# Kernel optimization log

Hardware: AMD Instinct MI355X
Metric: run time of the kernel (lower is better)

Reference implementation:

```python
import jax, jax.numpy as jnp
import numpy as np

DIM = 768
N_HEADS = 12
HEAD_DIM = DIM // N_HEADS  # 64
SEQ = 4096
ROPE_THETA = 10000.0  # local layer (layer_id=1)
WINDOW = 128          # local_attention; mask is distance <= WINDOW // 2


def setup_inputs() -> dict:
    key = jax.random.key(0)
    k1, k2, k3 = jax.random.split(key, 3)
    x = jax.random.normal(k1, (1, SEQ, DIM), dtype=jnp.float32)
    position_ids = jnp.arange(SEQ, dtype=jnp.int64 if jax.config.jax_enable_x64 else jnp.int32).reshape(1, SEQ)
    wqkv = jax.random.normal(k2, (3 * DIM, DIM), dtype=jnp.float32) * 0.02
    wo = jax.random.normal(k3, (DIM, DIM), dtype=jnp.float32) * 0.02
    return {"x": x, "position_ids": position_ids, "wqkv": wqkv, "wo": wo}


def _rope_cos_sin(position_ids):
    # inv_freq over even dims, freqs duplicated to full head_dim
    inv_freq = 1.0 / (ROPE_THETA ** (jnp.arange(0, HEAD_DIM, 2, dtype=jnp.float32) / HEAD_DIM))
    pos = position_ids.reshape(-1).astype(jnp.float32)           # [S]
    freqs = pos[:, None] * inv_freq[None, :]                      # [S, hd/2]
    freqs = jnp.concatenate([freqs, freqs], axis=-1)              # [S, hd]
    return jnp.cos(freqs)[None, None], jnp.sin(freqs)[None, None]  # [1,1,S,hd]


def _rotate_half(t):
    h = t.shape[-1] // 2
    return jnp.concatenate([-t[..., h:], t[..., :h]], axis=-1)


def reference(x, position_ids, wqkv, wo):
    bsz, seq_len, _ = x.shape
    qkv = jnp.einsum("bsd,ed->bse", x, wqkv)                      # [B,S,3*dim]
    qkv = qkv.reshape(bsz, seq_len, 3, N_HEADS, HEAD_DIM)
    qkv = jnp.transpose(qkv, (0, 3, 2, 1, 4))                      # [B,H,3,S,hd]
    q, k, v = qkv[:, :, 0], qkv[:, :, 1], qkv[:, :, 2]             # [B,H,S,hd]

    cos, sin = _rope_cos_sin(position_ids)
    q = q * cos + _rotate_half(q) * sin
    k = k * cos + _rotate_half(k) * sin

    scale = HEAD_DIM ** -0.5
    scores = jnp.einsum("bhqd,bhkd->bhqk", q, k) * scale           # [B,H,S,S]

    # sliding-window mask: |i - j| <= WINDOW // 2
    idx = jnp.arange(seq_len)
    dist = jnp.abs(idx[None, :] - idx[:, None])                    # [S,S]
    window_mask = dist <= (WINDOW // 2)
    scores = jnp.where(window_mask[None, None], scores, -jnp.inf)

    attn = jax.nn.softmax(scores, axis=-1)
    out = jnp.einsum("bhqk,bhkd->bhqd", attn, v)                   # [B,H,S,hd]
    out = jnp.transpose(out, (0, 2, 1, 3)).reshape(bsz, seq_len, DIM)
    out = jnp.einsum("bsd,ed->bse", out, wo)
    return out
```

## Files before the change

### kernel.cpp

```cpp
#include <hip/hip_runtime.h>
#include <math.h>

#define SEQ 4096
#define DIM 768
#define NH 12
#define HD 64
#define QKV_N 2304
#define HALF_WIN 64

typedef __attribute__((ext_vector_type(8))) short bf16x8;
typedef __attribute__((ext_vector_type(4))) float floatx4;

__device__ __forceinline__ unsigned short f2bf(float f) {
    unsigned u = __float_as_uint(f);
    unsigned r = (u + 0x7fffu + ((u >> 16) & 1u)) >> 16;
    return (unsigned short)r;
}

__device__ __forceinline__ void gld16(const void* g, void* l) {
    __builtin_amdgcn_global_load_lds(
        (const __attribute__((address_space(1))) unsigned*)g,
        (__attribute__((address_space(3))) unsigned*)l, 16, 0, 0);
}

__device__ __forceinline__ void fast_sc(float x, float* s, float* c) {
    float r = x * 0.15915494309189535f;
    r = r - floorf(r);
    *s = __builtin_amdgcn_sinf(r);
    *c = __builtin_amdgcn_cosf(r);
}

__global__ __launch_bounds__(256) void cast3_bf16(const float* __restrict__ x,
                                                  const float* __restrict__ wqkv,
                                                  const float* __restrict__ wo,
                                                  unsigned short* __restrict__ dst,
                                                  int nx4, int nw4, int ntot4) {
    int i = blockIdx.x * 256 + threadIdx.x;
    if (i >= ntot4) return;
    const float4* src;
    int off;
    if (i < nx4)            { src = (const float4*)x;    off = i; }
    else if (i < nx4 + nw4) { src = (const float4*)wqkv; off = i - nx4; }
    else                    { src = (const float4*)wo;   off = i - nx4 - nw4; }
    float4 v = src[off];
    ushort4 r;
    r.x = f2bf(v.x); r.y = f2bf(v.y); r.z = f2bf(v.z); r.w = f2bf(v.w);
    *(ushort4*)(dst + (size_t)i * 4) = r;
}

__global__ __launch_bounds__(256) void gemm_qkv_rope(const unsigned short* __restrict__ A,
                                                     const unsigned short* __restrict__ B,
                                                     unsigned short* __restrict__ qr,
                                                     unsigned short* __restrict__ kr,
                                                     unsigned short* __restrict__ vt) {
    __shared__ __align__(16) short smem[16384];
    const int t  = threadIdx.x;
    const int wv = t >> 6, ln = t & 63;
    const int bm0 = blockIdx.y * 64;
    const int bn0 = blockIdx.x * 64;
    const int lrow = ln >> 3;
    const int lu   = ln & 7;
    const int frow = ln & 15;
    const int q    = ln >> 4;
    const int K = DIM;

    const unsigned short* gptr[4];
    int loff[4];
#pragma unroll
    for (int i = 0; i < 4; i++) {
        int idx = wv * 4 + i;
        int c   = (idx < 8) ? idx : idx - 8;
        int row = c * 8 + lrow;
        int g   = (lu ^ (row & 7)) << 3;
        if (idx < 8) {
            gptr[i] = A + (size_t)(bm0 + row) * K + g;
            loff[i] = c * 512;
        } else {
            gptr[i] = B + (size_t)(bn0 + row) * K + g;
            loff[i] = 4096 + c * 512;
        }
    }

    floatx4 acc[4];
#pragma unroll
    for (int j = 0; j < 4; j++) acc[j] = (floatx4){0.f, 0.f, 0.f, 0.f};

#pragma unroll
    for (int i = 0; i < 4; i++) gld16(gptr[i], (void*)(smem + loff[i]));
    __syncthreads();

    int cur = 0;
    for (int it = 0; it < 12; it++) {
        if (it + 1 < 12) {
            int nb = cur ^ 1;
            int k0n = (it + 1) * 64;
#pragma unroll
            for (int i = 0; i < 4; i++)
                gld16(gptr[i] + k0n, (void*)(smem + nb * 8192 + loff[i]));
        }
        short* As = smem + cur * 8192;
        short* Bs = As + 4096;
#pragma unroll
        for (int ks = 0; ks < 2; ks++) {
            bf16x8 af, bfr[4];
            {
                int ra = wv * 16 + frow;
                af = *(const bf16x8*)&As[ra * 64 + (((ks * 4 + q) ^ (ra & 7)) << 3)];
            }
#pragma unroll
            for (int nt = 0; nt < 4; nt++) {
                int rb = nt * 16 + frow;
                bfr[nt] = *(const bf16x8*)&Bs[rb * 64 + (((ks * 4 + q) ^ (rb & 7)) << 3)];
            }
#pragma unroll
            for (int nt = 0; nt < 4; nt++)
                acc[nt] = __builtin_amdgcn_mfma_f32_16x16x32_bf16(
                    af, bfr[nt], acc[nt], 0, 0, 0);
        }
        __syncthreads();
        cur ^= 1;
    }

    const int cn = frow;
    const int part = (bn0 >= 1536) ? 2 : (bn0 >= 768 ? 1 : 0);

    if (part < 2) {
        const int colw = bn0 - part * 768;
        const int h = colw >> 6;
        unsigned short* dst = (part == 0 ? qr : kr) + (size_t)h * SEQ * HD;
        const float invf0 = exp2f(-(float)cn * 0.4152410118609203f);
        const float invf1 = exp2f(-(float)(cn + 16) * 0.4152410118609203f);
        const int sbase = bm0 + wv * 16 + q * 4;
#pragma unroll
        for (int r = 0; r < 4; r++) {
            float ss = (float)(sbase + r);
            float sn0, cs0, sn1, cs1;
            fast_sc(ss * invf0, &sn0, &cs0);
            fast_sc(ss * invf1, &sn1, &cs1);
            float o0 = acc[0][r] * cs0 - acc[2][r] * sn0;
            float o1 = acc[1][r] * cs1 - acc[3][r] * sn1;
            float o2 = acc[2][r] * cs0 + acc[0][r] * sn0;
            float o3 = acc[3][r] * cs1 + acc[1][r] * sn1;
            unsigned short* p = dst + (size_t)(sbase + r) * HD + cn;
            p[0]  = f2bf(o0);
            p[16] = f2bf(o1);
            p[32] = f2bf(o2);
            p[48] = f2bf(o3);
        }
    } else {
        short* vstage = smem;
#pragma unroll
        for (int nt = 0; nt < 4; nt++) {
            int d    = nt * 16 + cn;
            int sloc = wv * 16 + q * 4;
            ushort4 pk;
            pk.x = f2bf(acc[nt][0]);
            pk.y = f2bf(acc[nt][1]);
            pk.z = f2bf(acc[nt][2]);
            pk.w = f2bf(acc[nt][3]);
            *(ushort4*)&vstage[d * 72 + sloc] = pk;
        }
        __syncthreads();
        const int dr = t >> 2, sh = (t & 3) * 16;
        const int vcol = bn0 - 1536 + dr;
        unsigned short* vp = vt + (size_t)vcol * SEQ + bm0 + sh;
        *(uint4*)(vp)     = *(const uint4*)&vstage[dr * 72 + sh];
        *(uint4*)(vp + 8) = *(const uint4*)&vstage[dr * 72 + sh + 8];
    }
}

__global__ __launch_bounds__(256) void gemm_out(const unsigned short* __restrict__ A,
                                                const unsigned short* __restrict__ B,
                                                float* __restrict__ C,
                                                int M, int N, int K) {
    __shared__ __align__(16) short smem[16384];
    const int t  = threadIdx.x;
    const int wv = t >> 6, ln = t & 63;
    const int wm = wv >> 1, wn = wv & 1;
    const int bm0 = blockIdx.y * 64;
    const int bn0 = blockIdx.x * 64;
    const int lrow = ln >> 3;
    const int lu   = ln & 7;
    const int frow = ln & 15;
    const int q    = ln >> 4;

    const unsigned short* gptr[4];
    int loff[4];
#pragma unroll
    for (int i = 0; i < 4; i++) {
        int idx = wv * 4 + i;
        int c   = (idx < 8) ? idx : idx - 8;
        int row = c * 8 + lrow;
        int g   = (lu ^ (row & 7)) << 3;
        if (idx < 8) {
            gptr[i] = A + (size_t)(bm0 + row) * K + g;
            loff[i] = c * 512;
        } else {
            gptr[i] = B + (size_t)(bn0 + row) * K + g;
            loff[i] = 4096 + c * 512;
        }
    }

    floatx4 acc[2][2];
#pragma unroll
    for (int i = 0; i < 2; i++)
#pragma unroll
        for (int j = 0; j < 2; j++) acc[i][j] = (floatx4){0.f, 0.f, 0.f, 0.f};

#pragma unroll
    for (int i = 0; i < 4; i++) gld16(gptr[i], (void*)(smem + loff[i]));
    __syncthreads();

    int cur = 0;
    const int NIT = K / 64;
    for (int it = 0; it < NIT; it++) {
        if (it + 1 < NIT) {
            int nb = cur ^ 1;
            int k0n = (it + 1) * 64;
#pragma unroll
            for (int i = 0; i < 4; i++)
                gld16(gptr[i] + k0n, (void*)(smem + nb * 8192 + loff[i]));
        }
        short* As = smem + cur * 8192;
        short* Bs = As + 4096;
#pragma unroll
        for (int ks = 0; ks < 2; ks++) {
            bf16x8 af[2], bfr[2];
#pragma unroll
            for (int mt = 0; mt < 2; mt++) {
                int ra = wm * 32 + mt * 16 + frow;
                af[mt] = *(const bf16x8*)&As[ra * 64 + (((ks * 4 + q) ^ (ra & 7)) << 3)];
            }
#pragma unroll
            for (int nt = 0; nt < 2; nt++) {
                int rb = wn * 32 + nt * 16 + frow;
                bfr[nt] = *(const bf16x8*)&Bs[rb * 64 + (((ks * 4 + q) ^ (rb & 7)) << 3)];
            }
#pragma unroll
            for (int mt = 0; mt < 2; mt++)
#pragma unroll
                for (int nt = 0; nt < 2; nt++)
                    acc[mt][nt] = __builtin_amdgcn_mfma_f32_16x16x32_bf16(
                        af[mt], bfr[nt], acc[mt][nt], 0, 0, 0);
        }
        __syncthreads();
        cur ^= 1;
    }

    const int cn = ln & 15;
    const int rb4 = (ln >> 4) * 4;
#pragma unroll
    for (int mt = 0; mt < 2; mt++) {
#pragma unroll
        for (int nt = 0; nt < 2; nt++) {
            floatx4 v = acc[mt][nt];
            float* cp = C + (size_t)(bm0 + wm * 32 + mt * 16 + rb4) * N +
                        bn0 + wn * 32 + nt * 16 + cn;
#pragma unroll
            for (int r = 0; r < 4; r++) cp[(size_t)r * N] = v[r];
        }
    }
}

__global__ __launch_bounds__(512) void attn_mfma(const unsigned short* __restrict__ Q,
                                                 const unsigned short* __restrict__ K,
                                                 const unsigned short* __restrict__ Vt,
                                                 unsigned short* __restrict__ Out) {
    __shared__ __align__(16) short lds[16384];
    short* Ks  = lds;
    short* Vts = lds + 4096;
    short* Pb  = lds + 8192;
    const int t  = threadIdx.x;
    const int wv = t >> 6, ln = t & 63;
    const int h  = blockIdx.x, qs = blockIdx.y * 128;
    const int frow = ln & 15, qd = ln >> 4;
    const int rl = ln >> 3, uu = ln & 7;
    const unsigned short* Qh = Q + (size_t)h * SEQ * HD;
    const unsigned short* Kh = K + (size_t)h * SEQ * HD;
    const unsigned short* Vh = Vt + (size_t)h * HD * SEQ;

    const unsigned short* qp = Qh + (size_t)(qs + wv * 16 + frow) * HD;
    bf16x8 af0 = *(const bf16x8*)(qp + qd * 8);
    bf16x8 af1 = *(const bf16x8*)(qp + (qd + 4) * 8);

    floatx4 accO[4];
#pragma unroll
    for (int i = 0; i < 4; i++) accO[i] = (floatx4){0.f, 0.f, 0.f, 0.f};
    float m_r[4] = {-1e30f, -1e30f, -1e30f, -1e30f};
    float l_r[4] = {0.f, 0.f, 0.f, 0.f};

    const int qlo = wv * 16;

    for (int c = 0; c < 4; c++) {
        const int kb  = qs - 64 + c * 64;
        const int kbc = kb < 0 ? 0 : (kb > SEQ - 64 ? SEQ - 64 : kb);
        __syncthreads();
        {
            int row = wv * 8 + rl;
            int g = uu ^ ((row + (row >> 3)) & 7);
            gld16(Kh + (size_t)(kbc + row) * HD + g * 8, (void*)(Ks + wv * 512));
            gld16(Vh + (size_t)row * SEQ + kbc + g * 8, (void*)(Vts + wv * 512));
        }
        __syncthreads();

        const int klo0 = c * 64 - 64;
        bool live_kt[4];
        bool any_live = false;
#pragma unroll
        for (int kt = 0; kt < 4; kt++) {
            int d0 = qlo - (klo0 + kt * 16);
            live_kt[kt] = (d0 <= 64) && (d0 >= -64);
            any_live = any_live || live_kt[kt];
        }

        float sv[4][4];
        float cm[4] = {-1e30f, -1e30f, -1e30f, -1e30f};
        if (any_live) {
#pragma unroll
            for (int kt = 0; kt < 4; kt++) {
                if (live_kt[kt]) {
                    int brow = kt * 16 + frow;
                    int bz = (brow + (brow >> 3)) & 7;
                    bf16x8 b0 = *(const bf16x8*)&Ks[brow * 64 + ((qd ^ bz) << 3)];
                    bf16x8 b1 = *(const bf16x8*)&Ks[brow * 64 + (((qd + 4) ^ bz) << 3)];
                    floatx4 z = (floatx4){0.f, 0.f, 0.f, 0.f};
                    z = __builtin_amdgcn_mfma_f32_16x16x32_bf16(af0, b0, z, 0, 0, 0);
                    z = __builtin_amdgcn_mfma_f32_16x16x32_bf16(af1, b1, z, 0, 0, 0);
                    int gk = kb + kt * 16 + frow;
#pragma unroll
                    for (int r = 0; r < 4; r++) {
                        int gq = qs + wv * 16 + qd * 4 + r;
                        int dd = gq - gk;
                        bool valid = (gk >= 0) && (gk < SEQ) &&
                                     (dd <= HALF_WIN) && (dd >= -HALF_WIN);
                        float x = valid ? z[r] * 0.125f : -1e30f;
                        sv[kt][r] = x;
                        cm[r] = fmaxf(cm[r], x);
                    }
                } else {
#pragma unroll
                    for (int r = 0; r < 4; r++) sv[kt][r] = -1e30f;
                }
            }
#pragma unroll
            for (int off = 1; off < 16; off <<= 1)
#pragma unroll
                for (int r = 0; r < 4; r++)
                    cm[r] = fmaxf(cm[r], __shfl_xor(cm[r], off, 64));
            float al[4], ls[4];
#pragma unroll
            for (int r = 0; r < 4; r++) {
                float mn = fmaxf(m_r[r], cm[r]);
                al[r] = __expf(m_r[r] - mn);
                m_r[r] = mn;
                ls[r] = 0.f;
            }
            const int qrb = wv * 16 + qd * 4;
#pragma unroll
            for (int kt = 0; kt < 4; kt++) {
                int klocal = kt * 16 + frow;
                int ku = klocal >> 3;
                if (live_kt[kt]) {
#pragma unroll
                    for (int r = 0; r < 4; r++) {
                        float p = (sv[kt][r] > -1e29f) ? __expf(sv[kt][r] - m_r[r]) : 0.f;
                        ls[r] += p;
                        int qrow = qrb + r;
                        int pz = (qrow + (qrow >> 3)) & 7;
                        Pb[qrow * 64 + ((ku ^ pz) << 3) + (klocal & 7)] = (short)f2bf(p);
                    }
                } else {
#pragma unroll
                    for (int r = 0; r < 4; r++) {
                        int qrow = qrb + r;
                        int pz = (qrow + (qrow >> 3)) & 7;
                        Pb[qrow * 64 + ((ku ^ pz) << 3) + (klocal & 7)] = 0;
                    }
                }
            }
#pragma unroll
            for (int off = 1; off < 16; off <<= 1)
#pragma unroll
                for (int r = 0; r < 4; r++) ls[r] += __shfl_xor(ls[r], off, 64);
#pragma unroll
            for (int r = 0; r < 4; r++) l_r[r] = l_r[r] * al[r] + ls[r];
#pragma unroll
            for (int dt = 0; dt < 4; dt++)
#pragma unroll
                for (int r = 0; r < 4; r++) accO[dt][r] *= al[r];
        }
        __syncthreads();

        if (any_live) {
            const int prow = wv * 16 + frow;
            const int pz2 = (prow + (prow >> 3)) & 7;
            bf16x8 pa0 = *(const bf16x8*)&Pb[prow * 64 + ((qd ^ pz2) << 3)];
            bf16x8 pa1 = *(const bf16x8*)&Pb[prow * 64 + (((qd + 4) ^ pz2) << 3)];
#pragma unroll
            for (int dt = 0; dt < 4; dt++) {
                int vrow = dt * 16 + frow;
                int vz = (vrow + (vrow >> 3)) & 7;
                bf16x8 v0 = *(const bf16x8*)&Vts[vrow * 64 + ((qd ^ vz) << 3)];
                bf16x8 v1 = *(const bf16x8*)&Vts[vrow * 64 + (((qd + 4) ^ vz) << 3)];
                accO[dt] = __builtin_amdgcn_mfma_f32_16x16x32_bf16(pa0, v0, accO[dt], 0, 0, 0);
                accO[dt] = __builtin_amdgcn_mfma_f32_16x16x32_bf16(pa1, v1, accO[dt], 0, 0, 0);
            }
        }
    }

    __syncthreads();
    short* Ob = lds;
    float linv[4];
#pragma unroll
    for (int r = 0; r < 4; r++) linv[r] = 1.0f / l_r[r];
#pragma unroll
    for (int dt = 0; dt < 4; dt++)
#pragma unroll
        for (int r = 0; r < 4; r++) {
            int qrow = wv * 16 + qd * 4 + r;
            int dcol = dt * 16 + frow;
            Ob[qrow * 72 + dcol] = (short)f2bf(accO[dt][r] * linv[r]);
        }
    __syncthreads();
    const int orow = t >> 2, og = (t & 3) * 16;
    uint4 a = *(const uint4*)&Ob[orow * 72 + og];
    uint4 b = *(const uint4*)&Ob[orow * 72 + og + 8];
    unsigned short* op = Out + (size_t)(qs + orow) * DIM + h * HD + og;
    *(uint4*)(op)     = a;
    *(uint4*)(op + 8) = b;
}

extern "C" void kernel_launch(void* const* d_in, const int* in_sizes, int n_in,
                              void* d_out, int out_size, void* d_ws, size_t ws_size,
                              hipStream_t stream) {
    const float* x    = (const float*)d_in[0];
    const float* wqkv = (const float*)d_in[2];
    const float* wo   = (const float*)d_in[3];
    float* out = (float*)d_out;

    unsigned short* q_r  = (unsigned short*)d_ws;
    unsigned short* k_r  = q_r + (size_t)NH * SEQ * HD;
    unsigned short* v_t  = k_r + (size_t)NH * SEQ * HD;
    unsigned short* x_bf = v_t + (size_t)NH * SEQ * HD;
    unsigned short* wqkv_bf = x_bf + (size_t)SEQ * DIM;
    unsigned short* wo_bf   = wqkv_bf + (size_t)QKV_N * DIM;
    unsigned short* attn_bf = wo_bf + (size_t)DIM * DIM;

    const int nx4 = SEQ * DIM / 4;
    const int nw4 = QKV_N * DIM / 4;
    const int no4 = DIM * DIM / 4;
    const int ntot4 = nx4 + nw4 + no4;

    cast3_bf16<<<dim3((ntot4 + 255) / 256), 256, 0, stream>>>(
        x, wqkv, wo, x_bf, nx4, nw4, ntot4);
    gemm_qkv_rope<<<dim3(QKV_N / 64, SEQ / 64), 256, 0, stream>>>(
        x_bf, wqkv_bf, q_r, k_r, v_t);
    attn_mfma<<<dim3(NH, SEQ / 128), 512, 0, stream>>>(
        q_r, k_r, v_t, attn_bf);
    gemm_out<<<dim3(DIM / 64, SEQ / 64), 256, 0, stream>>>(
        attn_bf, wo_bf, out, SEQ, DIM, DIM);
}
```

Baseline: 127.6 us.

## Enlarge QKV GEMM tile to 128x128 with 2x2 warp layout

The QKV+RoPE GEMM moves from 64x64 tiles to 128x128 tiles, with each wave computing a 64x64 sub-tile (4x4 MFMA accumulators). This raises arithmetic intensity and cuts redundant global loads of A and B. The LDS double-buffering is dropped in favour of a single buffer with a load-then-sync each iteration. The grid shrinks from 2304 to 576 blocks, which lowers parallelism on a large-CU GPU, uses more registers, and exposes load latency without the prefetch.

```diff
diff --git a/kernel.cpp b/kernel.cpp
--- a/kernel.cpp
+++ b/kernel.cpp
@@ -53,119 +53,126 @@
                                                      unsigned short* __restrict__ qr,
                                                      unsigned short* __restrict__ kr,
                                                      unsigned short* __restrict__ vt) {
-    __shared__ __align__(16) short smem[16384];
+    __shared__ __align__(16) short smem[18432];
     const int t  = threadIdx.x;
     const int wv = t >> 6, ln = t & 63;
-    const int bm0 = blockIdx.y * 64;
-    const int bn0 = blockIdx.x * 64;
+    const int wm = wv >> 1, wn = wv & 1;
+    const int bm0 = blockIdx.y * 128;
+    const int bn0 = blockIdx.x * 128;
     const int lrow = ln >> 3;
     const int lu   = ln & 7;
     const int frow = ln & 15;
     const int q    = ln >> 4;
     const int K = DIM;
 
-    const unsigned short* gptr[4];
-    int loff[4];
-#pragma unroll
-    for (int i = 0; i < 4; i++) {
-        int idx = wv * 4 + i;
-        int c   = (idx < 8) ? idx : idx - 8;
+    const unsigned short* gptr[8];
+    int loff[8];
+#pragma unroll
+    for (int i = 0; i < 8; i++) {
+        int idx = wv * 8 + i;
+        int c   = (idx < 16) ? idx : idx - 16;
         int row = c * 8 + lrow;
         int g   = (lu ^ (row & 7)) << 3;
-        if (idx < 8) {
+        if (idx < 16) {
             gptr[i] = A + (size_t)(bm0 + row) * K + g;
             loff[i] = c * 512;
         } else {
             gptr[i] = B + (size_t)(bn0 + row) * K + g;
-            loff[i] = 4096 + c * 512;
-        }
-    }
-
-    floatx4 acc[4];
-#pragma unroll
-    for (int j = 0; j < 4; j++) acc[j] = (floatx4){0.f, 0.f, 0.f, 0.f};
-
-#pragma unroll
-    for (int i = 0; i < 4; i++) gld16(gptr[i], (void*)(smem + loff[i]));
-    __syncthreads();
-
-    int cur = 0;
+            loff[i] = 8192 + c * 512;
+        }
+    }
+
+    floatx4 acc[4][4];
+#pragma unroll
+    for (int i = 0; i < 4; i++)
+#pragma unroll
+        for (int j = 0; j < 4; j++) acc[i][j] = (floatx4){0.f, 0.f, 0.f, 0.f};
+
+    short* As = smem;
+    short* Bs = smem + 8192;
     for (int it = 0; it < 12; it++) {
-        if (it + 1 < 12) {
-            int nb = cur ^ 1;
-            int k0n = (it + 1) * 64;
-#pragma unroll
-            for (int i = 0; i < 4; i++)
-                gld16(gptr[i] + k0n, (void*)(smem + nb * 8192 + loff[i]));
-        }
-        short* As = smem + cur * 8192;
-        short* Bs = As + 4096;
+        const int k0 = it * 64;
+#pragma unroll
+        for (int i = 0; i < 8; i++) gld16(gptr[i] + k0, (void*)(smem + loff[i]));
+        __syncthreads();
 #pragma unroll
         for (int ks = 0; ks < 2; ks++) {
-            bf16x8 af, bfr[4];
-            {
-                int ra = wv * 16 + frow;
-                af = *(const bf16x8*)&As[ra * 64 + (((ks * 4 + q) ^ (ra & 7)) << 3)];
+            bf16x8 af[4], bfr[4];
+#pragma unroll
+            for (int mt = 0; mt < 4; mt++) {
+                int ra = wm * 64 + mt * 16 + frow;
+                af[mt] = *(const bf16x8*)&As[ra * 64 + (((ks * 4 + q) ^ (ra & 7)) << 3)];
             }
 #pragma unroll
             for (int nt = 0; nt < 4; nt++) {
-                int rb = nt * 16 + frow;
+                int rb = wn * 64 + nt * 16 + frow;
                 bfr[nt] = *(const bf16x8*)&Bs[rb * 64 + (((ks * 4 + q) ^ (rb & 7)) << 3)];
             }
 #pragma unroll
-            for (int nt = 0; nt < 4; nt++)
-                acc[nt] = __builtin_amdgcn_mfma_f32_16x16x32_bf16(
-                    af, bfr[nt], acc[nt], 0, 0, 0);
-        }
-        __syncthreads();
-        cur ^= 1;
+            for (int mt = 0; mt < 4; mt++)
+#pragma unroll
+                for (int nt = 0; nt < 4; nt++)
+                    acc[mt][nt] = __builtin_amdgcn_mfma_f32_16x16x32_bf16(
+                        af[mt], bfr[nt], acc[mt][nt], 0, 0, 0);
+        }
+        __syncthreads();
     }
 
     const int cn = frow;
     const int part = (bn0 >= 1536) ? 2 : (bn0 >= 768 ? 1 : 0);
 
     if (part < 2) {
-        const int colw = bn0 - part * 768;
-        const int h = colw >> 6;
+        const int wcol = bn0 - part * 768 + wn * 64;
+        const int h = wcol >> 6;
         unsigned short* dst = (part == 0 ? qr : kr) + (size_t)h * SEQ * HD;
         const float invf0 = exp2f(-(float)cn * 0.4152410118609203f);
         const float invf1 = exp2f(-(float)(cn + 16) * 0.4152410118609203f);
-        const int sbase = bm0 + wv * 16 + q * 4;
-#pragma unroll
-        for (int r = 0; r < 4; r++) {
-            float ss = (float)(sbase + r);
-            float sn0, cs0, sn1, cs1;
-            fast_sc(ss * invf0, &sn0, &cs0);
-            fast_sc(ss * invf1, &sn1, &cs1);
-            float o0 = acc[0][r] * cs0 - acc[2][r] * sn0;
-            float o1 = acc[1][r] * cs1 - acc[3][r] * sn1;
-            float o2 = acc[2][r] * cs0 + acc[0][r] * sn0;
-            float o3 = acc[3][r] * cs1 + acc[1][r] * sn1;
-            unsigned short* p = dst + (size_t)(sbase + r) * HD + cn;
-            p[0]  = f2bf(o0);
-            p[16] = f2bf(o1);
-            p[32] = f2bf(o2);
-            p[48] = f2bf(o3);
+#pragma unroll
+        for (int mt = 0; mt < 4; mt++) {
+            const int sbase = bm0 + wm * 64 + mt * 16 + q * 4;
+#pragma unroll
+            for (int r = 0; r < 4; r++) {
+                float ss = (float)(sbase + r);
+                float sn0, cs0, sn1, cs1;
+                fast_sc(ss * invf0, &sn0, &cs0);
+                fast_sc(ss * invf1, &sn1, &cs1);
+                float o0 = acc[mt][0][r] * cs0 - acc[mt][2][r] * sn0;
+                float o1 = acc[mt][1][r] * cs1 - acc[mt][3][r] * sn1;
+                float o2 = acc[mt][2][r] * cs0 + acc[mt][0][r] * sn0;
+                float o3 = acc[mt][3][r] * cs1 + acc[mt][1][r] * sn1;
+                unsigned short* p = dst + (size_t)(sbase + r) * HD + cn;
+                p[0]  = f2bf(o0);
+                p[16] = f2bf(o1);
+                p[32] = f2bf(o2);
+                p[48] = f2bf(o3);
+            }
         }
     } else {
-        short* vstage = smem;
-#pragma unroll
-        for (int nt = 0; nt < 4; nt++) {
-            int d    = nt * 16 + cn;
-            int sloc = wv * 16 + q * 4;
-            ushort4 pk;
-            pk.x = f2bf(acc[nt][0]);
-            pk.y = f2bf(acc[nt][1]);
-            pk.z = f2bf(acc[nt][2]);
-            pk.w = f2bf(acc[nt][3]);
-            *(ushort4*)&vstage[d * 72 + sloc] = pk;
-        }
-        __syncthreads();
-        const int dr = t >> 2, sh = (t & 3) * 16;
-        const int vcol = bn0 - 1536 + dr;
-        unsigned short* vp = vt + (size_t)vcol * SEQ + bm0 + sh;
-        *(uint4*)(vp)     = *(const uint4*)&vstage[dr * 72 + sh];
-        *(uint4*)(vp + 8) = *(const uint4*)&vstage[dr * 72 + sh + 8];
+        short* vstage = smem + wv * 4608;
+#pragma unroll
+        for (int mt = 0; mt < 4; mt++) {
+#pragma unroll
+            for (int nt = 0; nt < 4; nt++) {
+                int d    = nt * 16 + cn;
+                int sloc = mt * 16 + q * 4;
+                ushort4 pk;
+                pk.x = f2bf(acc[mt][nt][0]);
+                pk.y = f2bf(acc[mt][nt][1]);
+                pk.z = f2bf(acc[mt][nt][2]);
+                pk.w = f2bf(acc[mt][nt][3]);
+                *(ushort4*)&vstage[d * 72 + sloc] = pk;
+            }
+        }
+        __syncthreads();
+#pragma unroll
+        for (int itr = 0; itr < 8; itr++) {
+            int dr = (t >> 4) + itr * 16;
+            int u  = t & 15;
+            int region = ((u >> 3) << 1) | (dr >> 6);
+            uint4 val = *(const uint4*)&smem[region * 4608 + (dr & 63) * 72 + (u & 7) * 8];
+            unsigned short* vp = vt + (size_t)(bn0 - 1536 + dr) * SEQ + bm0 + u * 8;
+            *(uint4*)vp = val;
+        }
     }
 }
 
@@ -453,7 +460,7 @@
 
     cast3_bf16<<<dim3((ntot4 + 255) / 256), 256, 0, stream>>>(
         x, wqkv, wo, x_bf, nx4, nw4, ntot4);
-    gemm_qkv_rope<<<dim3(QKV_N / 64, SEQ / 64), 256, 0, stream>>>(
+    gemm_qkv_rope<<<dim3(QKV_N / 128, SEQ / 128), 256, 0, stream>>>(
         x_bf, wqkv_bf, q_r, k_r, v_t);
     attn_mfma<<<dim3(NH, SEQ / 128), 512, 0, stream>>>(
         q_r, k_r, v_t, attn_bf);
```

New measurement: 136.3 us. +6.8%, slower.
